# Optimization experiments

Measured on AMD Instinct MI355X. Metric: run time of the kernel, lower is better.

## Reference

```python
import jax, jax.numpy as jnp
import numpy as np

N, C, H, NG = 200000, 256, 4, 512
D = C // H  # head_dim = 64


def setup_inputs() -> dict:
    key = jax.random.key(0)
    ks = jax.random.split(key, 10)
    s = 1.0 / np.sqrt(C)
    inp = {
        "x": jax.random.normal(ks[0], (N, C), dtype=jnp.float32),
        "batch": jnp.sort(jax.random.randint(ks[1], (N,), 0, NG)),
        "Wq": jax.random.uniform(ks[2], (C, C), jnp.float32, -s, s),
        "bq": jnp.zeros((C,), jnp.float32),
        "Wk": jax.random.uniform(ks[3], (C, C), jnp.float32, -s, s),
        "bk": jnp.zeros((C,), jnp.float32),
        "Wv": jax.random.uniform(ks[4], (C, C), jnp.float32, -s, s),
        "bv": jnp.zeros((C,), jnp.float32),
        "Wo": jax.random.uniform(ks[5], (C, C), jnp.float32, -s, s),
        "bo": jnp.zeros((C,), jnp.float32),
    }
    return inp


def reference(x, batch, Wq, bq, Wk, bk, Wv, bv, Wo, bo):
    n = x.shape[0]
    q = (x @ Wq + bq).reshape(n, H, D)
    k = (x @ Wk + bk).reshape(n, H, D)
    v = (x @ Wv + bv).reshape(n, H, D)
    # per-node head-vs-head scores: [N, H, H]
    scores = jnp.einsum("nhd,ngd->nhg", q, k) / jnp.sqrt(jnp.float32(D))
    # segment softmax across nodes within each graph (torch_geometric.utils.softmax)
    seg_max = jax.ops.segment_max(scores, batch, num_segments=NG)
    e = jnp.exp(scores - seg_max[batch])
    seg_sum = jax.ops.segment_sum(e, batch, num_segments=NG)
    att = e / (seg_sum[batch] + 1e-16)
    out = jnp.einsum("nhg,ngd->nhd", att, v).reshape(n, C)
    out = out @ Wo + bo
    return (out, att.mean(axis=1))
```

## Files before the change

### kernel.cpp

```cpp
#include <hip/hip_runtime.h>

#define NN 200000
#define CC 256
#define NG 512

typedef __attribute__((ext_vector_type(8))) __bf16 bf16x8;
typedef __attribute__((ext_vector_type(16))) float f32x16;

typedef unsigned short u16;

__device__ __forceinline__ u16 f2bf(float f) {
  union { float f; unsigned u; } v; v.f = f;
  unsigned u = v.u;
  u += 0x7fffu + ((u >> 16) & 1u);
  return (u16)(u >> 16);
}
__device__ __forceinline__ unsigned pack2(float a, float b) {
  return (unsigned)f2bf(a) | ((unsigned)f2bf(b) << 16);
}
__device__ __forceinline__ float bflo(unsigned u){ union{unsigned u; float f;} x; x.u = u << 16; return x.f; }
__device__ __forceinline__ float bfhi(unsigned u){ union{unsigned u; float f;} x; x.u = u & 0xffff0000u; return x.f; }

__global__ __launch_bounds__(256) void prep_kernel(
    const float* __restrict__ Wq, const float* __restrict__ Wk,
    const float* __restrict__ Wv, const float* __restrict__ Wo,
    u16* __restrict__ Wall) {
  int idx = blockIdx.x * 256 + threadIdx.x;
  int s = idx >> 13;
  int inner = idx & 8191;
  int ks = inner >> 9;
  int l = (inner >> 3) & 63;
  int j = inner & 7;
  int r = l & 31, hi5 = l >> 5;
  int k = ks * 16 + hi5 * 8 + j;
  const float* W; int c0;
  if (s < 16) {
    int p = s >> 3, r4 = s & 7;
    if (r4 < 4) { W = Wk; c0 = r4 * 64 + p * 32; }
    else        { W = Wq; c0 = (r4 - 4) * 64 + p * 32; }
  } else if (s < 24) { W = Wv; c0 = (s - 16) * 32; }
  else               { W = Wo; c0 = (s - 24) * 32; }
  Wall[idx] = f2bf(W[k * 256 + c0 + r]);
}

__global__ __launch_bounds__(256) void seg_bounds_kernel(
    const int* __restrict__ batch, int* __restrict__ seg_start, int n) {
  int i = blockIdx.x * 256 + threadIdx.x;
  if (i >= n) return;
  int a = batch[i];
  int b = (i + 1 < n) ? batch[i + 1] : NG;
  for (int g = a + 1; g <= b; ++g) seg_start[g] = i + 1;
  if (i == 0) for (int g = 0; g <= a; ++g) seg_start[g] = 0;
}

__device__ __forceinline__ void stage_slice(
    const u16* __restrict__ Wall, u16* dst_base, int s, int w, int lane) {
#pragma unroll
  for (int rep = 0; rep < 4; ++rep) {
    const u16* src = Wall + (size_t)s * 8192 + ((w * 4 + rep) * 64 + lane) * 8;
    u16* dst = dst_base + (w * 4 + rep) * 512;
    __builtin_amdgcn_global_load_lds(
        (const __attribute__((address_space(1))) void*)src,
        (__attribute__((address_space(3))) void*)dst, 16, 0, 0);
  }
}

__device__ __forceinline__ f32x16 gemm_lds(
    const u16* buf, const bf16x8 xfr[16], int lane) {
  f32x16 a0 = {0.f,0.f,0.f,0.f,0.f,0.f,0.f,0.f,0.f,0.f,0.f,0.f,0.f,0.f,0.f,0.f};
  f32x16 a1 = a0;
#pragma unroll
  for (int ks = 0; ks < 16; ks += 2) {
    bf16x8 f0 = *reinterpret_cast<const bf16x8*>(&buf[(ks * 64 + lane) * 8]);
    bf16x8 f1 = *reinterpret_cast<const bf16x8*>(&buf[((ks + 1) * 64 + lane) * 8]);
    a0 = __builtin_amdgcn_mfma_f32_32x32x16_bf16(f0, xfr[ks], a0, 0, 0, 0);
    a1 = __builtin_amdgcn_mfma_f32_32x32x16_bf16(f1, xfr[ks + 1], a1, 0, 0, 0);
  }
  return a0 + a1;
}

__global__ __launch_bounds__(256, 2) void qkv_scores_kernel(
    const float* __restrict__ x, const u16* __restrict__ Wall,
    const float* __restrict__ bq, const float* __restrict__ bk,
    const float* __restrict__ bv,
    u16* __restrict__ v_out,
    float* __restrict__ scores) {
  __shared__ u16 Wbuf[2][8192];

  const int t = threadIdx.x;
  const int w = t >> 6, lane = t & 63;
  const int col = lane & 31, hi5 = lane >> 5;
  const int n = blockIdx.x * 128 + w * 32 + col;
  const int nl = (n < NN) ? n : (NN - 1);
  const bool valid = (n < NN);

  stage_slice(Wall, Wbuf[0], 0, w, lane);

  bf16x8 xfr[16];
#pragma unroll
  for (int kb = 0; kb < 16; ++kb) {
    const float* px = x + (size_t)nl * CC + kb * 16 + hi5 * 8;
    float4 a0 = *reinterpret_cast<const float4*>(px);
    float4 a1 = *reinterpret_cast<const float4*>(px + 4);
    uint4 u = {pack2(a0.x, a0.y), pack2(a0.z, a0.w),
               pack2(a1.x, a1.y), pack2(a1.z, a1.w)};
    xfr[kb] = *reinterpret_cast<bf16x8*>(&u);
  }
  __syncthreads();

  float sp[16];
#pragma unroll
  for (int i = 0; i < 16; ++i) sp[i] = 0.f;

#pragma unroll 1
  for (int p = 0; p < 2; ++p) {
    unsigned kph[4][8];
#pragma unroll
    for (int g = 0; g < 4; ++g) {
      stage_slice(Wall, Wbuf[(g + 1) & 1], p * 8 + g + 1, w, lane);
      f32x16 acc = gemm_lds(Wbuf[g & 1], xfr, lane);
#pragma unroll
      for (int q = 0; q < 4; ++q) {
        float4 b4 = *reinterpret_cast<const float4*>(
            bk + g * 64 + p * 32 + q * 8 + hi5 * 4);
        kph[g][q * 2]     = pack2(acc[4 * q] + b4.x, acc[4 * q + 1] + b4.y);
        kph[g][q * 2 + 1] = pack2(acc[4 * q + 2] + b4.z, acc[4 * q + 3] + b4.w);
      }
      __syncthreads();
    }
#pragma unroll
    for (int h = 0; h < 4; ++h) {
      stage_slice(Wall, Wbuf[(h + 1) & 1], p * 8 + 5 + h, w, lane);
      f32x16 acc = gemm_lds(Wbuf[h & 1], xfr, lane);
#pragma unroll
      for (int q = 0; q < 4; ++q) {
        float4 b4 = *reinterpret_cast<const float4*>(
            bq + h * 64 + p * 32 + q * 8 + hi5 * 4);
        float q0 = acc[4 * q] + b4.x, q1 = acc[4 * q + 1] + b4.y;
        float q2 = acc[4 * q + 2] + b4.z, q3 = acc[4 * q + 3] + b4.w;
#pragma unroll
        for (int g = 0; g < 4; ++g) {
          unsigned k01 = kph[g][q * 2];
          unsigned k23 = kph[g][q * 2 + 1];
          sp[h * 4 + g] += q0 * bflo(k01) + q1 * bfhi(k01) +
                           q2 * bflo(k23) + q3 * bfhi(k23);
        }
      }
      __syncthreads();
    }
  }

#pragma unroll
  for (int i = 0; i < 16; ++i) sp[i] += __shfl_xor(sp[i], 32, 64);
  if (hi5 == 0 && valid) {
#pragma unroll
    for (int q = 0; q < 4; ++q) {
      float4 o = {sp[q * 4] * 0.125f, sp[q * 4 + 1] * 0.125f,
                  sp[q * 4 + 2] * 0.125f, sp[q * 4 + 3] * 0.125f};
      *reinterpret_cast<float4*>(scores + (size_t)n * 16 + q * 4) = o;
    }
  }

#pragma unroll
  for (int sv = 0; sv < 8; ++sv) {
    if (sv < 7) stage_slice(Wall, Wbuf[(sv + 1) & 1], 17 + sv, w, lane);
    f32x16 acc = gemm_lds(Wbuf[sv & 1], xfr, lane);
    if (valid) {
#pragma unroll
      for (int q = 0; q < 4; ++q) {
        int d0 = sv * 32 + q * 8 + hi5 * 4;
        float4 b4 = *reinterpret_cast<const float4*>(bv + d0);
        uint2 pk = {pack2(acc[4 * q] + b4.x, acc[4 * q + 1] + b4.y),
                    pack2(acc[4 * q + 2] + b4.z, acc[4 * q + 3] + b4.w)};
        *reinterpret_cast<uint2*>(v_out + (size_t)n * CC + d0) = pk;
      }
    }
    __syncthreads();
  }
}

__global__ __launch_bounds__(256) void seg_softmax_kernel(
    const float* __restrict__ scores, const int* __restrict__ seg_start,
    float* __restrict__ seg_max, float* __restrict__ seg_sum) {
  __shared__ float red[256];
  int g = blockIdx.x;
  int s = seg_start[g], e = seg_start[g + 1];
  int t = threadIdx.x;
  int col = t & 15, sub = t >> 4;

  float m = -INFINITY;
  for (int i = s + sub; i < e; i += 16)
    m = fmaxf(m, scores[(size_t)i * 16 + col]);
  red[t] = m;
  __syncthreads();
  for (int step = 8; step >= 1; step >>= 1) {
    if (sub < step) red[t] = fmaxf(red[t], red[t + step * 16]);
    __syncthreads();
  }
  if (t < 16) seg_max[g * 16 + t] = red[t];
  float mcol = red[col];
  __syncthreads();

  float sum = 0.f;
  for (int i = s + sub; i < e; i += 16)
    sum += expf(scores[(size_t)i * 16 + col] - mcol);
  red[t] = sum;
  __syncthreads();
  for (int step = 8; step >= 1; step >>= 1) {
    if (sub < step) red[t] += red[t + step * 16];
    __syncthreads();
  }
  if (t < 16) seg_sum[g * 16 + t] = red[t];
}

__global__ __launch_bounds__(256, 2) void out_kernel(
    const u16* __restrict__ v_bf, const float* __restrict__ scores,
    const int* __restrict__ batch, const float* __restrict__ seg_max,
    const float* __restrict__ seg_sum, const u16* __restrict__ Wall,
    const float* __restrict__ bo, float* __restrict__ out,
    float* __restrict__ att_mean) {
  __shared__ u16 Wbuf[2][8192];

  const int t = threadIdx.x;
  const int w = t >> 6, lane = t & 63;
  const int col = lane & 31, hi5 = lane >> 5;
  const int n = blockIdx.x * 128 + w * 32 + col;
  const int nl = (n < NN) ? n : (NN - 1);
  const bool valid = (n < NN);

  stage_slice(Wall, Wbuf[0], 24, w, lane);

  int b = batch[nl];
  float att[16];
#pragma unroll
  for (int q = 0; q < 4; ++q) {
    float4 sc = *reinterpret_cast<const float4*>(scores + (size_t)nl * 16 + q * 4);
    float4 mx = *reinterpret_cast<const float4*>(seg_max + b * 16 + q * 4);
    float4 sm = *reinterpret_cast<const float4*>(seg_sum + b * 16 + q * 4);
    att[q * 4 + 0] = expf(sc.x - mx.x) / (sm.x + 1e-16f);
    att[q * 4 + 1] = expf(sc.y - mx.y) / (sm.y + 1e-16f);
    att[q * 4 + 2] = expf(sc.z - mx.z) / (sm.z + 1e-16f);
    att[q * 4 + 3] = expf(sc.w - mx.w) / (sm.w + 1e-16f);
  }
  if (hi5 == 0 && valid) {
    float4 am;
    am.x = 0.25f * (att[0] + att[4] + att[8] + att[12]);
    am.y = 0.25f * (att[1] + att[5] + att[9] + att[13]);
    am.z = 0.25f * (att[2] + att[6] + att[10] + att[14]);
    am.w = 0.25f * (att[3] + att[7] + att[11] + att[15]);
    *reinterpret_cast<float4*>(att_mean + (size_t)n * 4) = am;
  }

  bf16x8 oaf[16];
#pragma unroll
  for (int dw = 0; dw < 4; ++dw) {
    int dd = dw * 16 + hi5 * 8;
    float vr[4][8];
#pragma unroll
    for (int g = 0; g < 4; ++g) {
      uint4 vv = *reinterpret_cast<const uint4*>(
          v_bf + (size_t)nl * CC + g * 64 + dd);
      vr[g][0] = bflo(vv.x); vr[g][1] = bfhi(vv.x);
      vr[g][2] = bflo(vv.y); vr[g][3] = bfhi(vv.y);
      vr[g][4] = bflo(vv.z); vr[g][5] = bfhi(vv.z);
      vr[g][6] = bflo(vv.w); vr[g][7] = bfhi(vv.w);
    }
#pragma unroll
    for (int h = 0; h < 4; ++h) {
      unsigned res[4];
#pragma unroll
      for (int jj = 0; jj < 4; ++jj) {
        float lo = att[h * 4 + 0] * vr[0][2 * jj] + att[h * 4 + 1] * vr[1][2 * jj] +
                   att[h * 4 + 2] * vr[2][2 * jj] + att[h * 4 + 3] * vr[3][2 * jj];
        float hf = att[h * 4 + 0] * vr[0][2 * jj + 1] + att[h * 4 + 1] * vr[1][2 * jj + 1] +
                   att[h * 4 + 2] * vr[2][2 * jj + 1] + att[h * 4 + 3] * vr[3][2 * jj + 1];
        res[jj] = pack2(lo, hf);
      }
      uint4 u = {res[0], res[1], res[2], res[3]};
      oaf[h * 4 + dw] = *reinterpret_cast<bf16x8*>(&u);
    }
  }
  __syncthreads();

#pragma unroll
  for (int so = 0; so < 8; ++so) {
    if (so < 7) stage_slice(Wall, Wbuf[(so + 1) & 1], 25 + so, w, lane);
    f32x16 acc = gemm_lds(Wbuf[so & 1], oaf, lane);
    if (valid) {
#pragma unroll
      for (int q = 0; q < 4; ++q) {
        int c0 = so * 32 + q * 8 + hi5 * 4;
        float4 b4 = *reinterpret_cast<const float4*>(bo + c0);
        float4 o = {acc[4 * q] + b4.x, acc[4 * q + 1] + b4.y,
                    acc[4 * q + 2] + b4.z, acc[4 * q + 3] + b4.w};
        *reinterpret_cast<float4*>(out + (size_t)n * CC + c0) = o;
      }
    }
    __syncthreads();
  }
}

extern "C" void kernel_launch(void* const* d_in, const int* in_sizes, int n_in,
                              void* d_out, int out_size, void* d_ws, size_t ws_size,
                              hipStream_t stream) {
  const float* x  = (const float*)d_in[0];
  const int* batch = (const int*)d_in[1];
  const float* Wq = (const float*)d_in[2];
  const float* bq = (const float*)d_in[3];
  const float* Wk = (const float*)d_in[4];
  const float* bk = (const float*)d_in[5];
  const float* Wv = (const float*)d_in[6];
  const float* bv = (const float*)d_in[7];
  const float* Wo = (const float*)d_in[8];
  const float* bo = (const float*)d_in[9];

  char* ws = (char*)d_ws;
  u16*   Wall      = (u16*)ws;
  int*   seg_start = (int*)(ws + 524288);
  float* seg_max   = (float*)(ws + 528384);
  float* seg_sum   = (float*)(ws + 561152);
  float* scores    = (float*)(ws + 593920);
  u16*   v_bf      = (u16*)(ws + 13393920);

  float* out = (float*)d_out;
  float* att_mean = out + (size_t)NN * CC;

  const int NB = (NN + 127) / 128;

  prep_kernel<<<1024, 256, 0, stream>>>(Wq, Wk, Wv, Wo, Wall);
  seg_bounds_kernel<<<(NN + 255) / 256, 256, 0, stream>>>(batch, seg_start, NN);
  qkv_scores_kernel<<<NB, 256, 0, stream>>>(x, Wall, bq, bk, bv, v_bf, scores);
  seg_softmax_kernel<<<NG, 256, 0, stream>>>(scores, seg_start, seg_max, seg_sum);
  out_kernel<<<NB, 256, 0, stream>>>(v_bf, scores, batch, seg_max, seg_sum,
                                     Wall, bo, out, att_mean);
}
```

Baseline: 290.4 us.

## Prefetch two weight slices ahead with explicit vmcnt waits and raise occupancy

Replaces the per-slice __syncthreads double-buffer scheme with a two-deep prefetch. Slices s and s+1 are staged up front, and after each slice's GEMM its buffer is refilled with slice s+2, guarded by explicit s_waitcnt vmcnt counts, raw s_barrier and sched_barrier fences. The out kernel also hoists all V loads ahead of the weight staging, and both kernels raise launch_bounds min-blocks from 2 to 4. The aim is to hide global-to-LDS weight latency and cut barrier stalls. The cost is fragile hand-counted vmcnt values that depend on the stores and loads the compiler emits, plus register pressure from full unrolling and the higher occupancy target.

Measured after the change: 751.6 us. +158.8%, slower.

```diff
diff --git a/kernel.cpp b/kernel.cpp
--- a/kernel.cpp
+++ b/kernel.cpp
@@ -8,6 +8,10 @@
 typedef __attribute__((ext_vector_type(16))) float f32x16;
 
 typedef unsigned short u16;
+
+#define VWAITN(n) asm volatile("s_waitcnt vmcnt(%0)" :: "i"(n) : "memory")
+#define SBAR() __builtin_amdgcn_s_barrier()
+#define SCHED() __builtin_amdgcn_sched_barrier(0)
 
 __device__ __forceinline__ u16 f2bf(float f) {
   union { float f; unsigned u; } v; v.f = f;
@@ -79,7 +83,7 @@
   return a0 + a1;
 }
 
-__global__ __launch_bounds__(256, 2) void qkv_scores_kernel(
+__global__ __launch_bounds__(256, 4) void qkv_scores_kernel(
     const float* __restrict__ x, const u16* __restrict__ Wall,
     const float* __restrict__ bq, const float* __restrict__ bk,
     const float* __restrict__ bv,
@@ -95,6 +99,7 @@
   const bool valid = (n < NN);
 
   stage_slice(Wall, Wbuf[0], 0, w, lane);
+  SCHED();
 
   bf16x8 xfr[16];
 #pragma unroll
@@ -106,19 +111,25 @@
                pack2(a1.x, a1.y), pack2(a1.z, a1.w)};
     xfr[kb] = *reinterpret_cast<bf16x8*>(&u);
   }
-  __syncthreads();
+  SCHED();
+  stage_slice(Wall, Wbuf[1], 1, w, lane);
+  SCHED();
 
   float sp[16];
 #pragma unroll
   for (int i = 0; i < 16; ++i) sp[i] = 0.f;
 
-#pragma unroll 1
+#pragma unroll
   for (int p = 0; p < 2; ++p) {
     unsigned kph[4][8];
 #pragma unroll
     for (int g = 0; g < 4; ++g) {
-      stage_slice(Wall, Wbuf[(g + 1) & 1], p * 8 + g + 1, w, lane);
-      f32x16 acc = gemm_lds(Wbuf[g & 1], xfr, lane);
+      const int sl = p * 8 + g;
+      VWAITN(4);
+      SBAR(); SCHED();
+      f32x16 acc = gemm_lds(Wbuf[sl & 1], xfr, lane);
+      SCHED(); SBAR();
+      stage_slice(Wall, Wbuf[sl & 1], sl + 2, w, lane);
 #pragma unroll
       for (int q = 0; q < 4; ++q) {
         float4 b4 = *reinterpret_cast<const float4*>(
@@ -126,12 +137,15 @@
         kph[g][q * 2]     = pack2(acc[4 * q] + b4.x, acc[4 * q + 1] + b4.y);
         kph[g][q * 2 + 1] = pack2(acc[4 * q + 2] + b4.z, acc[4 * q + 3] + b4.w);
       }
-      __syncthreads();
     }
 #pragma unroll
     for (int h = 0; h < 4; ++h) {
-      stage_slice(Wall, Wbuf[(h + 1) & 1], p * 8 + 5 + h, w, lane);
-      f32x16 acc = gemm_lds(Wbuf[h & 1], xfr, lane);
+      const int sl = p * 8 + 4 + h;
+      VWAITN(4);
+      SBAR(); SCHED();
+      f32x16 acc = gemm_lds(Wbuf[sl & 1], xfr, lane);
+      SCHED(); SBAR();
+      stage_slice(Wall, Wbuf[sl & 1], sl + 2, w, lane);
 #pragma unroll
       for (int q = 0; q < 4; ++q) {
         float4 b4 = *reinterpret_cast<const float4*>(
@@ -146,7 +160,6 @@
                            q2 * bflo(k23) + q3 * bfhi(k23);
         }
       }
-      __syncthreads();
     }
   }
 
@@ -163,8 +176,14 @@
 
 #pragma unroll
   for (int sv = 0; sv < 8; ++sv) {
-    if (sv < 7) stage_slice(Wall, Wbuf[(sv + 1) & 1], 17 + sv, w, lane);
-    f32x16 acc = gemm_lds(Wbuf[sv & 1], xfr, lane);
+    const int sl = 16 + sv;
+    if (sv == 0)      { VWAITN(4); }
+    else if (sv < 7)  { VWAITN(8); }
+    else              { VWAITN(4); }
+    SBAR(); SCHED();
+    f32x16 acc = gemm_lds(Wbuf[sl & 1], xfr, lane);
+    SCHED(); SBAR();
+    if (sv < 6) stage_slice(Wall, Wbuf[sl & 1], sl + 2, w, lane);
     if (valid) {
 #pragma unroll
       for (int q = 0; q < 4; ++q) {
@@ -175,7 +194,6 @@
         *reinterpret_cast<uint2*>(v_out + (size_t)n * CC + d0) = pk;
       }
     }
-    __syncthreads();
   }
 }
 
@@ -213,7 +231,7 @@
   if (t < 16) seg_sum[g * 16 + t] = red[t];
 }
 
-__global__ __launch_bounds__(256, 2) void out_kernel(
+__global__ __launch_bounds__(256, 4) void out_kernel(
     const u16* __restrict__ v_bf, const float* __restrict__ scores,
     const int* __restrict__ batch, const float* __restrict__ seg_max,
     const float* __restrict__ seg_sum, const u16* __restrict__ Wall,
@@ -227,8 +245,6 @@
   const int n = blockIdx.x * 128 + w * 32 + col;
   const int nl = (n < NN) ? n : (NN - 1);
   const bool valid = (n < NN);
-
-  stage_slice(Wall, Wbuf[0], 24, w, lane);
 
   int b = batch[nl];
   float att[16];
@@ -242,6 +258,20 @@
     att[q * 4 + 2] = expf(sc.z - mx.z) / (sm.z + 1e-16f);
     att[q * 4 + 3] = expf(sc.w - mx.w) / (sm.w + 1e-16f);
   }
+
+  uint4 vv[4][4];
+#pragma unroll
+  for (int g = 0; g < 4; ++g)
+#pragma unroll
+    for (int dw = 0; dw < 4; ++dw)
+      vv[g][dw] = *reinterpret_cast<const uint4*>(
+          v_bf + (size_t)nl * CC + g * 64 + dw * 16 + hi5 * 8);
+
+  stage_slice(Wall, Wbuf[0], 24, w, lane);
+  SCHED();
+  stage_slice(Wall, Wbuf[1], 25, w, lane);
+  SCHED();
+
   if (hi5 == 0 && valid) {
     float4 am;
     am.x = 0.25f * (att[0] + att[4] + att[8] + att[12]);
@@ -254,16 +284,14 @@
   bf16x8 oaf[16];
 #pragma unroll
   for (int dw = 0; dw < 4; ++dw) {
-    int dd = dw * 16 + hi5 * 8;
     float vr[4][8];
 #pragma unroll
     for (int g = 0; g < 4; ++g) {
-      uint4 vv = *reinterpret_cast<const uint4*>(
-          v_bf + (size_t)nl * CC + g * 64 + dd);
-      vr[g][0] = bflo(vv.x); vr[g][1] = bfhi(vv.x);
-      vr[g][2] = bflo(vv.y); vr[g][3] = bfhi(vv.y);
-      vr[g][4] = bflo(vv.z); vr[g][5] = bfhi(vv.z);
-      vr[g][6] = bflo(vv.w); vr[g][7] = bfhi(vv.w);
+      uint4 u4 = vv[g][dw];
+      vr[g][0] = bflo(u4.x); vr[g][1] = bfhi(u4.x);
+      vr[g][2] = bflo(u4.y); vr[g][3] = bfhi(u4.y);
+      vr[g][4] = bflo(u4.z); vr[g][5] = bfhi(u4.z);
+      vr[g][6] = bflo(u4.w); vr[g][7] = bfhi(u4.w);
     }
 #pragma unroll
     for (int h = 0; h < 4; ++h) {
@@ -280,12 +308,16 @@
       oaf[h * 4 + dw] = *reinterpret_cast<bf16x8*>(&u);
     }
   }
-  __syncthreads();
 
 #pragma unroll
   for (int so = 0; so < 8; ++so) {
-    if (so < 7) stage_slice(Wall, Wbuf[(so + 1) & 1], 25 + so, w, lane);
+    if (so == 0)      { VWAITN(4); }
+    else if (so < 7)  { VWAITN(8); }
+    else              { VWAITN(4); }
+    SBAR(); SCHED();
     f32x16 acc = gemm_lds(Wbuf[so & 1], oaf, lane);
+    SCHED(); SBAR();
+    if (so < 6) stage_slice(Wall, Wbuf[so & 1], 26 + so, w, lane);
     if (valid) {
 #pragma unroll
       for (int q = 0; q < 4; ++q) {
@@ -296,7 +328,6 @@
         *reinterpret_cast<float4*>(out + (size_t)n * CC + c0) = o;
       }
     }
-    __syncthreads();
   }
 }
 
```

## Stage x loads, V and output stores through LDS for coalesced global access

Applied to the files above, without the earlier changes.

x is now loaded cooperatively with row-contiguous coalesced reads, converted to bf16 and written into a swizzled LDS layout before being pulled into MFMA fragments. The V intermediate is restaged through LDS and written in a slice-major [8][N][32] layout with full 16-byte rows, which out_kernel reads back coalesced into LDS. The final fp32 output is also staged through LDS so that each so-slice is stored as contiguous row chunks, and biases are cached in shared memory. This replaces strided per-lane global accesses with coalesced ones, at the cost of more LDS traffic, extra barriers, and larger shared memory (64-70KB), which may reduce occupancy.

After: 320.3 us. 10.3% more time.

```diff
diff --git a/kernel.cpp b/kernel.cpp
--- a/kernel.cpp
+++ b/kernel.cpp
@@ -6,7 +6,6 @@
 
 typedef __attribute__((ext_vector_type(8))) __bf16 bf16x8;
 typedef __attribute__((ext_vector_type(16))) float f32x16;
-
 typedef unsigned short u16;
 
 __device__ __forceinline__ u16 f2bf(float f) {
@@ -83,67 +82,85 @@
     const float* __restrict__ x, const u16* __restrict__ Wall,
     const float* __restrict__ bq, const float* __restrict__ bk,
     const float* __restrict__ bv,
-    u16* __restrict__ v_out,
+    u16* __restrict__ v_bf,
     float* __restrict__ scores) {
-  __shared__ u16 Wbuf[2][8192];
+  __shared__ __align__(16) char smem[65536];
+  u16* xs = (u16*)smem;
+  u16 (*Wbuf)[8192] = (u16(*)[8192])smem;
+  u16* Vst = (u16*)(smem + 32768);
+  float* biasL = (float*)(smem + 53248);
 
   const int t = threadIdx.x;
   const int w = t >> 6, lane = t & 63;
   const int col = lane & 31, hi5 = lane >> 5;
-  const int n = blockIdx.x * 128 + w * 32 + col;
-  const int nl = (n < NN) ? n : (NN - 1);
+  const int r0 = blockIdx.x * 128;
+  const int node = w * 32 + col;
+  const int n = r0 + node;
   const bool valid = (n < NN);
 
+#pragma unroll
+  for (int i = 0; i < 16; ++i) {
+    int u = i * 256 + t;
+    int r = u >> 5, c8 = (u & 31) * 8;
+    int gr = r0 + r; if (gr >= NN) gr = NN - 1;
+    const float* px = x + (size_t)gr * CC + c8;
+    float4 a0 = *(const float4*)px;
+    float4 a1 = *(const float4*)(px + 4);
+    uint4 pk = {pack2(a0.x, a0.y), pack2(a0.z, a0.w),
+                pack2(a1.x, a1.y), pack2(a1.z, a1.w)};
+    int kb = c8 >> 4, hi = (c8 >> 3) & 1;
+    int lp = (hi * 32 + (r & 31)) ^ kb;
+    *(uint4*)&xs[(((r >> 5) * 16 + kb) * 64 + lp) * 8] = pk;
+  }
+  __syncthreads();
+
+  bf16x8 xfr[16];
+#pragma unroll
+  for (int kb = 0; kb < 16; ++kb)
+    xfr[kb] = *(const bf16x8*)&xs[((w * 16 + kb) * 64 + (lane ^ kb)) * 8];
+  __syncthreads();
+
   stage_slice(Wall, Wbuf[0], 0, w, lane);
-
-  bf16x8 xfr[16];
-#pragma unroll
-  for (int kb = 0; kb < 16; ++kb) {
-    const float* px = x + (size_t)nl * CC + kb * 16 + hi5 * 8;
-    float4 a0 = *reinterpret_cast<const float4*>(px);
-    float4 a1 = *reinterpret_cast<const float4*>(px + 4);
-    uint4 u = {pack2(a0.x, a0.y), pack2(a0.z, a0.w),
-               pack2(a1.x, a1.y), pack2(a1.z, a1.w)};
-    xfr[kb] = *reinterpret_cast<bf16x8*>(&u);
-  }
+  biasL[t] = bk[t];
+  biasL[256 + t] = bq[t];
+  biasL[512 + t] = bv[t];
   __syncthreads();
 
   float sp[16];
 #pragma unroll
   for (int i = 0; i < 16; ++i) sp[i] = 0.f;
 
-#pragma unroll 1
+#pragma unroll
   for (int p = 0; p < 2; ++p) {
     unsigned kph[4][8];
 #pragma unroll
     for (int g = 0; g < 4; ++g) {
-      stage_slice(Wall, Wbuf[(g + 1) & 1], p * 8 + g + 1, w, lane);
-      f32x16 acc = gemm_lds(Wbuf[g & 1], xfr, lane);
+      const int sl = p * 8 + g;
+      stage_slice(Wall, Wbuf[(sl + 1) & 1], sl + 1, w, lane);
+      f32x16 acc = gemm_lds(Wbuf[sl & 1], xfr, lane);
 #pragma unroll
       for (int q = 0; q < 4; ++q) {
-        float4 b4 = *reinterpret_cast<const float4*>(
-            bk + g * 64 + p * 32 + q * 8 + hi5 * 4);
-        kph[g][q * 2]     = pack2(acc[4 * q] + b4.x, acc[4 * q + 1] + b4.y);
-        kph[g][q * 2 + 1] = pack2(acc[4 * q + 2] + b4.z, acc[4 * q + 3] + b4.w);
+        float4 b4 = *(const float4*)&biasL[g * 64 + p * 32 + q * 8 + hi5 * 4];
+        kph[g][q * 2]     = pack2(acc[4*q] + b4.x, acc[4*q+1] + b4.y);
+        kph[g][q * 2 + 1] = pack2(acc[4*q+2] + b4.z, acc[4*q+3] + b4.w);
       }
       __syncthreads();
     }
 #pragma unroll
     for (int h = 0; h < 4; ++h) {
-      stage_slice(Wall, Wbuf[(h + 1) & 1], p * 8 + 5 + h, w, lane);
-      f32x16 acc = gemm_lds(Wbuf[h & 1], xfr, lane);
+      const int sl = p * 8 + 4 + h;
+      stage_slice(Wall, Wbuf[(sl + 1) & 1], sl + 1, w, lane);
+      f32x16 acc = gemm_lds(Wbuf[sl & 1], xfr, lane);
 #pragma unroll
       for (int q = 0; q < 4; ++q) {
-        float4 b4 = *reinterpret_cast<const float4*>(
-            bq + h * 64 + p * 32 + q * 8 + hi5 * 4);
-        float q0 = acc[4 * q] + b4.x, q1 = acc[4 * q + 1] + b4.y;
-        float q2 = acc[4 * q + 2] + b4.z, q3 = acc[4 * q + 3] + b4.w;
+        float4 b4 = *(const float4*)&biasL[256 + h * 64 + p * 32 + q * 8 + hi5 * 4];
+        float q0 = acc[4*q] + b4.x, q1 = acc[4*q+1] + b4.y;
+        float q2 = acc[4*q+2] + b4.z, q3 = acc[4*q+3] + b4.w;
 #pragma unroll
         for (int g = 0; g < 4; ++g) {
-          unsigned k01 = kph[g][q * 2];
-          unsigned k23 = kph[g][q * 2 + 1];
-          sp[h * 4 + g] += q0 * bflo(k01) + q1 * bfhi(k01) +
-                           q2 * bflo(k23) + q3 * bfhi(k23);
+          unsigned k01 = kph[g][q * 2], k23 = kph[g][q * 2 + 1];
+          sp[h*4+g] += q0 * bflo(k01) + q1 * bfhi(k01) +
+                       q2 * bflo(k23) + q3 * bfhi(k23);
         }
       }
       __syncthreads();
@@ -155,9 +172,9 @@
   if (hi5 == 0 && valid) {
 #pragma unroll
     for (int q = 0; q < 4; ++q) {
-      float4 o = {sp[q * 4] * 0.125f, sp[q * 4 + 1] * 0.125f,
-                  sp[q * 4 + 2] * 0.125f, sp[q * 4 + 3] * 0.125f};
-      *reinterpret_cast<float4*>(scores + (size_t)n * 16 + q * 4) = o;
+      float4 o = {sp[q*4] * 0.125f, sp[q*4+1] * 0.125f,
+                  sp[q*4+2] * 0.125f, sp[q*4+3] * 0.125f};
+      *(float4*)(scores + (size_t)n * 16 + q * 4) = o;
     }
   }
 
@@ -165,17 +182,26 @@
   for (int sv = 0; sv < 8; ++sv) {
     if (sv < 7) stage_slice(Wall, Wbuf[(sv + 1) & 1], 17 + sv, w, lane);
     f32x16 acc = gemm_lds(Wbuf[sv & 1], xfr, lane);
-    if (valid) {
-#pragma unroll
-      for (int q = 0; q < 4; ++q) {
-        int d0 = sv * 32 + q * 8 + hi5 * 4;
-        float4 b4 = *reinterpret_cast<const float4*>(bv + d0);
-        uint2 pk = {pack2(acc[4 * q] + b4.x, acc[4 * q + 1] + b4.y),
-                    pack2(acc[4 * q + 2] + b4.z, acc[4 * q + 3] + b4.w)};
-        *reinterpret_cast<uint2*>(v_out + (size_t)n * CC + d0) = pk;
+    u16* vb = Vst + (sv & 1) * 5120;
+#pragma unroll
+    for (int q = 0; q < 4; ++q) {
+      float4 b4 = *(const float4*)&biasL[512 + sv * 32 + q * 8 + hi5 * 4];
+      uint2 pk = {pack2(acc[4*q] + b4.x, acc[4*q+1] + b4.y),
+                  pack2(acc[4*q+2] + b4.z, acc[4*q+3] + b4.w)};
+      *(uint2*)&vb[node * 40 + q * 8 + hi5 * 4] = pk;
+    }
+    __syncthreads();
+    {
+      int rr = t >> 1, h2 = t & 1;
+      uint4 d0 = *(const uint4*)&vb[rr * 40 + h2 * 16];
+      uint4 d1 = *(const uint4*)&vb[rr * 40 + h2 * 16 + 8];
+      int gn = r0 + rr;
+      if (gn < NN) {
+        u16* dst = v_bf + ((size_t)sv * NN + gn) * 32 + h2 * 16;
+        *(uint4*)dst = d0;
+        *(uint4*)(dst + 8) = d1;
       }
     }
-    __syncthreads();
   }
 }
 
@@ -219,28 +245,42 @@
     const float* __restrict__ seg_sum, const u16* __restrict__ Wall,
     const float* __restrict__ bo, float* __restrict__ out,
     float* __restrict__ att_mean) {
-  __shared__ u16 Wbuf[2][8192];
+  __shared__ __align__(16) char smem[70656];
+  u16* vs = (u16*)smem;
+  u16 (*Wbuf)[8192] = (u16(*)[8192])smem;
+  float* ostage = (float*)(smem + 32768);
+  float* boL = (float*)(smem + 69632);
 
   const int t = threadIdx.x;
   const int w = t >> 6, lane = t & 63;
   const int col = lane & 31, hi5 = lane >> 5;
-  const int n = blockIdx.x * 128 + w * 32 + col;
+  const int r0 = blockIdx.x * 128;
+  const int node = w * 32 + col;
+  const int n = r0 + node;
   const int nl = (n < NN) ? n : (NN - 1);
   const bool valid = (n < NN);
 
-  stage_slice(Wall, Wbuf[0], 24, w, lane);
+#pragma unroll
+  for (int i = 0; i < 16; ++i) {
+    int u = i * 256 + t;
+    int sv = u >> 9, iu = u & 511;
+    int nd = iu >> 2, dp = (iu & 3) * 8;
+    int gn = r0 + nd; if (gn >= NN) gn = NN - 1;
+    uint4 d = *(const uint4*)&v_bf[((size_t)sv * NN + gn) * 32 + dp];
+    *(uint4*)&vs[nd * 264 + sv * 32 + dp] = d;
+  }
 
   int b = batch[nl];
   float att[16];
 #pragma unroll
   for (int q = 0; q < 4; ++q) {
-    float4 sc = *reinterpret_cast<const float4*>(scores + (size_t)nl * 16 + q * 4);
-    float4 mx = *reinterpret_cast<const float4*>(seg_max + b * 16 + q * 4);
-    float4 sm = *reinterpret_cast<const float4*>(seg_sum + b * 16 + q * 4);
-    att[q * 4 + 0] = expf(sc.x - mx.x) / (sm.x + 1e-16f);
-    att[q * 4 + 1] = expf(sc.y - mx.y) / (sm.y + 1e-16f);
-    att[q * 4 + 2] = expf(sc.z - mx.z) / (sm.z + 1e-16f);
-    att[q * 4 + 3] = expf(sc.w - mx.w) / (sm.w + 1e-16f);
+    float4 sc = *(const float4*)(scores + (size_t)nl * 16 + q * 4);
+    float4 mx = *(const float4*)(seg_max + b * 16 + q * 4);
+    float4 sm = *(const float4*)(seg_sum + b * 16 + q * 4);
+    att[q*4+0] = expf(sc.x - mx.x) / (sm.x + 1e-16f);
+    att[q*4+1] = expf(sc.y - mx.y) / (sm.y + 1e-16f);
+    att[q*4+2] = expf(sc.z - mx.z) / (sm.z + 1e-16f);
+    att[q*4+3] = expf(sc.w - mx.w) / (sm.w + 1e-16f);
   }
   if (hi5 == 0 && valid) {
     float4 am;
@@ -248,32 +288,31 @@
     am.y = 0.25f * (att[1] + att[5] + att[9] + att[13]);
     am.z = 0.25f * (att[2] + att[6] + att[10] + att[14]);
     am.w = 0.25f * (att[3] + att[7] + att[11] + att[15]);
-    *reinterpret_cast<float4*>(att_mean + (size_t)n * 4) = am;
-  }
+    *(float4*)(att_mean + (size_t)n * 4) = am;
+  }
+  __syncthreads();
 
   bf16x8 oaf[16];
 #pragma unroll
   for (int dw = 0; dw < 4; ++dw) {
-    int dd = dw * 16 + hi5 * 8;
     float vr[4][8];
 #pragma unroll
     for (int g = 0; g < 4; ++g) {
-      uint4 vv = *reinterpret_cast<const uint4*>(
-          v_bf + (size_t)nl * CC + g * 64 + dd);
-      vr[g][0] = bflo(vv.x); vr[g][1] = bfhi(vv.x);
-      vr[g][2] = bflo(vv.y); vr[g][3] = bfhi(vv.y);
-      vr[g][4] = bflo(vv.z); vr[g][5] = bfhi(vv.z);
-      vr[g][6] = bflo(vv.w); vr[g][7] = bfhi(vv.w);
+      uint4 u4 = *(const uint4*)&vs[node * 264 + g * 64 + dw * 16 + hi5 * 8];
+      vr[g][0] = bflo(u4.x); vr[g][1] = bfhi(u4.x);
+      vr[g][2] = bflo(u4.y); vr[g][3] = bfhi(u4.y);
+      vr[g][4] = bflo(u4.z); vr[g][5] = bfhi(u4.z);
+      vr[g][6] = bflo(u4.w); vr[g][7] = bfhi(u4.w);
     }
 #pragma unroll
     for (int h = 0; h < 4; ++h) {
       unsigned res[4];
 #pragma unroll
       for (int jj = 0; jj < 4; ++jj) {
-        float lo = att[h * 4 + 0] * vr[0][2 * jj] + att[h * 4 + 1] * vr[1][2 * jj] +
-                   att[h * 4 + 2] * vr[2][2 * jj] + att[h * 4 + 3] * vr[3][2 * jj];
-        float hf = att[h * 4 + 0] * vr[0][2 * jj + 1] + att[h * 4 + 1] * vr[1][2 * jj + 1] +
-                   att[h * 4 + 2] * vr[2][2 * jj + 1] + att[h * 4 + 3] * vr[3][2 * jj + 1];
+        float lo = att[h*4+0]*vr[0][2*jj]   + att[h*4+1]*vr[1][2*jj] +
+                   att[h*4+2]*vr[2][2*jj]   + att[h*4+3]*vr[3][2*jj];
+        float hf = att[h*4+0]*vr[0][2*jj+1] + att[h*4+1]*vr[1][2*jj+1] +
+                   att[h*4+2]*vr[2][2*jj+1] + att[h*4+3]*vr[3][2*jj+1];
         res[jj] = pack2(lo, hf);
       }
       uint4 u = {res[0], res[1], res[2], res[3]};
@@ -282,21 +321,32 @@
   }
   __syncthreads();
 
+  stage_slice(Wall, Wbuf[0], 24, w, lane);
+  boL[t] = bo[t];
+  __syncthreads();
+
 #pragma unroll
   for (int so = 0; so < 8; ++so) {
     if (so < 7) stage_slice(Wall, Wbuf[(so + 1) & 1], 25 + so, w, lane);
     f32x16 acc = gemm_lds(Wbuf[so & 1], oaf, lane);
-    if (valid) {
-#pragma unroll
-      for (int q = 0; q < 4; ++q) {
-        int c0 = so * 32 + q * 8 + hi5 * 4;
-        float4 b4 = *reinterpret_cast<const float4*>(bo + c0);
-        float4 o = {acc[4 * q] + b4.x, acc[4 * q + 1] + b4.y,
-                    acc[4 * q + 2] + b4.z, acc[4 * q + 3] + b4.w};
-        *reinterpret_cast<float4*>(out + (size_t)n * CC + c0) = o;
-      }
+    float* ob = ostage + (so & 1) * 4608;
+#pragma unroll
+    for (int q = 0; q < 4; ++q) {
+      float4 b4 = *(const float4*)&boL[so * 32 + q * 8 + hi5 * 4];
+      float4 o = {acc[4*q] + b4.x, acc[4*q+1] + b4.y,
+                  acc[4*q+2] + b4.z, acc[4*q+3] + b4.w};
+      *(float4*)&ob[node * 36 + q * 8 + hi5 * 4] = o;
     }
     __syncthreads();
+#pragma unroll
+    for (int i = 0; i < 4; ++i) {
+      int u = i * 256 + t;
+      int nd = u >> 3, part = u & 7;
+      float4 d = *(const float4*)&ob[nd * 36 + part * 4];
+      int gn = r0 + nd;
+      if (gn < NN)
+        *(float4*)&out[(size_t)gn * CC + so * 32 + part * 4] = d;
+    }
   }
 }
 
```
